# Optimization experiments

Measured on AMD Instinct MI355X. Metric: run time of the kernel, lower is better.

The kernel has to match this reference:

```python
import jax, jax.numpy as jnp
import numpy as np

WINDOW = 128  # crop size (compute_crops default window_size)


def centre_crop(centroids, window_size, h, w):
    # centroids: [C,2] int; returns flat gather coords [2, C*ws*ws]
    half = window_size // 2
    cy = jnp.clip(centroids[:, 0], half, h - half)
    cx = jnp.clip(centroids[:, 1], half, w - half)
    gy, gx = jnp.meshgrid(jnp.arange(window_size), jnp.arange(window_size), indexing='ij')
    rows = (cy - half)[:, None, None] + gy[None]  # [C,ws,ws]
    cols = (cx - half)[:, None, None] + gx[None]
    return jnp.stack([rows.reshape(-1), cols.reshape(-1)])  # [2, C*ws*ws]


def setup_inputs() -> dict:
    key = jax.random.key(0)
    ks = jax.random.split(key, 8)
    E, S, C, H, W = 6, 1, 512, 1024, 1024
    Dh = 16
    return {
        'x': jax.random.normal(ks[0], (E, H, W), dtype=jnp.float32),
        'sigma': jax.random.uniform(ks[1], (S, H, W), dtype=jnp.float32),
        'c': jax.random.normal(ks[2], (C, E), dtype=jnp.float32),
        'W1': jax.random.normal(ks[3], (E + S, Dh), dtype=jnp.float32) * 0.3,
        'b1': jnp.zeros((Dh,), dtype=jnp.float32),
        'W2': jax.random.normal(ks[4], (Dh, Dh), dtype=jnp.float32) * 0.3,
        'b2': jnp.zeros((Dh,), dtype=jnp.float32),
        'W3': jax.random.normal(ks[5], (Dh, 1), dtype=jnp.float32) * 0.3,
        'b3': jnp.zeros((1,), dtype=jnp.float32),
        'centroids_idx': jax.random.randint(ks[6], (C, 2), 0, H, dtype=jnp.int32),
    }


def reference(x, sigma, c, W1, b1, W2, b2, W3, b3, centroids_idx):
    E, h, w = x.shape
    S = sigma.shape[0]
    C = c.shape[0]
    ws = WINDOW
    mesh = centre_crop(centroids_idx, ws, h, w)  # [2, C*ws*ws]
    # gather per-instance windows from concatenated embedding+sigma maps
    xs = jnp.concatenate([x, sigma], axis=0)  # [E+S, H, W]
    g = xs[:, mesh[0], mesh[1]]               # [E+S, C*ws*ws]
    g = g.reshape(E + S, C, ws, ws).transpose(1, 0, 2, 3)  # [C, E+S, ws, ws]
    # subtract centroid descriptor from embedding channels (feature_engineering '0')
    g = jnp.concatenate([g[:, :E] - c[:, :, None, None], g[:, E:]], axis=1)
    feats = g.transpose(0, 2, 3, 1).reshape(-1, E + S)  # [(C*ws*ws), E+S]
    # per-pixel probability MLP (ProbabilityNet)
    hdn = jax.nn.relu(feats @ W1 + b1)
    hdn = jax.nn.relu(hdn @ W2 + b2)
    prob = jax.nn.sigmoid(hdn @ W3 + b3)
    prob = prob.reshape(C, 1, ws, ws)
    # instance-id / coordinate table for the downstream scatter (iidd)
    inst = jnp.repeat(jnp.arange(C, dtype=mesh.dtype), ws * ws)
    iidd = jnp.concatenate([inst[None], mesh], axis=0)  # [3, C*ws*ws]
    return prob, iidd
```

## Files before the change

### kernel.cpp

```cpp
#include <hip/hip_runtime.h>

#define WS 128
#define HW (1024 * 1024)
#define PLANE 8388608

typedef _Float16 half4 __attribute__((ext_vector_type(4)));
typedef _Float16 half8 __attribute__((ext_vector_type(8)));
typedef float floatx4 __attribute__((ext_vector_type(4)));

__global__ __launch_bounds__(256) void precompute_P(
    const float* __restrict__ x,
    const float* __restrict__ sigma,
    const float* __restrict__ W1,
    _Float16* __restrict__ P)
{
    const int px = blockIdx.x * 256 + threadIdx.x;
    float g[7];
#pragma unroll
    for (int e = 0; e < 6; ++e) g[e] = x[e * HW + px];
    g[6] = sigma[px];

    half8 lo, hi;
#pragma unroll
    for (int j = 0; j < 16; ++j) {
        float a = 0.0f;
#pragma unroll
        for (int e = 0; e < 7; ++e)
            a = fmaf(g[e], W1[e * 16 + j], a);
        if (j < 8) lo[j] = (_Float16)a; else hi[j - 8] = (_Float16)a;
    }
    *(half8*)(P + (size_t)px * 16)     = lo;
    *(half8*)(P + (size_t)px * 16 + 8) = hi;
}

__global__ __launch_bounds__(256) void instanseg_mlp(
    const _Float16* __restrict__ P,
    const float* __restrict__ c,
    const float* __restrict__ W1,
    const float* __restrict__ b1,
    const float* __restrict__ W2,
    const float* __restrict__ b2,
    const float* __restrict__ W3,
    const float* __restrict__ b3,
    const int*   __restrict__ cent,
    float* __restrict__ out)
{
    const int cid  = blockIdx.y;
    const int lane = threadIdx.x & 63;
    const int wave = threadIdx.x >> 6;
    const int quad = lane >> 4;
    const int sub  = lane & 15;

    const int cy = min(max(cent[2 * cid], 64), 960);
    const int cx = min(max(cent[2 * cid + 1], 64), 960);
    const int cy0 = cy - 64, cx0 = cx - 64;

    half4 a2;
    float w3f[4], bb2[4];
    half4 qh;
#pragma unroll
    for (int i = 0; i < 4; ++i) {
        const int k = 4 * quad + i;
        a2[i]  = (_Float16)W2[k * 16 + sub];
        w3f[i] = W3[k];
        bb2[i] = b2[k];
        float qv = -b1[k];
#pragma unroll
        for (int e = 0; e < 6; ++e)
            qv = fmaf(W1[e * 16 + k], c[cid * 6 + e], qv);
        qh[i] = (_Float16)qv;
    }
    const float b3v = b3[0];
    const floatx4 zero = {0.0f, 0.0f, 0.0f, 0.0f};

    const int wavestart = blockIdx.x * 2048 + wave * 512;

    for (int it = 0; it < 8; ++it) {
        const int start = wavestart + it * 64;
        float logit[4];
#pragma unroll
        for (int ch = 0; ch < 4; ++ch) {
            const int gp  = start + ch * 16 + sub;
            const int src = (cy0 + (gp >> 7)) * 1024 + cx0 + (gp & 127);

            half4 v = *(const half4*)(P + (size_t)src * 16 + quad * 4);
            half4 h = v - qh;
#pragma unroll
            for (int i = 0; i < 4; ++i)
                h[i] = h[i] > (_Float16)0.0f ? h[i] : (_Float16)0.0f;

            floatx4 c2 = __builtin_amdgcn_mfma_f32_16x16x16f16(a2, h, zero, 0, 0, 0);

            float part = 0.0f;
#pragma unroll
            for (int i = 0; i < 4; ++i)
                part = fmaf(w3f[i], fmaxf(c2[i] + bb2[i], 0.0f), part);
            part += __shfl_xor(part, 16, 64);
            part += __shfl_xor(part, 32, 64);
            logit[ch] = part;
        }

        const float l01 = (quad & 1) ? logit[1] : logit[0];
        const float l23 = (quad & 1) ? logit[3] : logit[2];
        const float lg  = (quad & 2) ? l23 : l01;
        const float prob = 1.0f / (1.0f + __expf(-(lg + b3v)));

        const int gps = start + lane;
        const int n   = cid * 16384 + gps;
        out[n]             = prob;
        out[PLANE + n]     = (float)cid;
        out[2 * PLANE + n] = (float)(cy0 + (gps >> 7));
        out[3 * PLANE + n] = (float)(cx0 + (gps & 127));
    }
}

extern "C" void kernel_launch(void* const* d_in, const int* in_sizes, int n_in,
                              void* d_out, int out_size, void* d_ws, size_t ws_size,
                              hipStream_t stream) {
    const float* x     = (const float*)d_in[0];
    const float* sigma = (const float*)d_in[1];
    const float* c     = (const float*)d_in[2];
    const float* W1    = (const float*)d_in[3];
    const float* b1    = (const float*)d_in[4];
    const float* W2    = (const float*)d_in[5];
    const float* b2    = (const float*)d_in[6];
    const float* W3    = (const float*)d_in[7];
    const float* b3    = (const float*)d_in[8];
    const int*   cent  = (const int*)d_in[9];
    float* out = (float*)d_out;
    _Float16* P = (_Float16*)d_ws;

    precompute_P<<<dim3(HW / 256), dim3(256), 0, stream>>>(x, sigma, W1, P);
    instanseg_mlp<<<dim3(8, 512), dim3(256), 0, stream>>>(
        P, c, W1, b1, W2, b2, W3, b3, cent, out);
}
```

Measured before the change: 211.8 us.

## Reorder crop blocks by Morton-sorted centroids for cache locality

An extra block added to the precompute kernel computes a Z-order key for each clamped centroid and ranks the 512 instances with an O(n^2) counting sort in shared memory. The MLP kernel now uses a 1D grid that maps each block to a sorted rank, interleaved across 8 groups, so spatially nearby crops run at about the same time and can share their P gathers in L2/MALL. The cost is the serial ranking block, which can lengthen the first kernel's tail, plus one extra indirection load per block. Output indexing still uses the original cid, so results stay correct.

```diff
diff --git a/kernel.cpp b/kernel.cpp
--- a/kernel.cpp
+++ b/kernel.cpp
@@ -3,17 +3,50 @@
 #define WS 128
 #define HW (1024 * 1024)
 #define PLANE 8388608
+#define PERM_BYTE_OFF 33554432
 
 typedef _Float16 half4 __attribute__((ext_vector_type(4)));
 typedef _Float16 half8 __attribute__((ext_vector_type(8)));
 typedef float floatx4 __attribute__((ext_vector_type(4)));
 
+__device__ inline unsigned part1by1(unsigned v) {
+    v &= 0x0000ffff;
+    v = (v ^ (v << 8)) & 0x00ff00ff;
+    v = (v ^ (v << 4)) & 0x0f0f0f0f;
+    v = (v ^ (v << 2)) & 0x33333333;
+    v = (v ^ (v << 1)) & 0x55555555;
+    return v;
+}
+
 __global__ __launch_bounds__(256) void precompute_P(
     const float* __restrict__ x,
     const float* __restrict__ sigma,
     const float* __restrict__ W1,
-    _Float16* __restrict__ P)
+    const int*   __restrict__ cent,
+    _Float16* __restrict__ P,
+    int* __restrict__ perm)
 {
+    if (blockIdx.x == 4096) {
+        __shared__ unsigned keys[512];
+        const int t = threadIdx.x;
+        for (int i = t; i < 512; i += 256) {
+            const unsigned cy = (unsigned)min(max(cent[2 * i], 64), 960);
+            const unsigned cx = (unsigned)min(max(cent[2 * i + 1], 64), 960);
+            keys[i] = (part1by1(cy) << 1) | part1by1(cx);
+        }
+        __syncthreads();
+        for (int i = t; i < 512; i += 256) {
+            const unsigned ki = keys[i];
+            int r = 0;
+            for (int j = 0; j < 512; ++j) {
+                const unsigned kj = keys[j];
+                r += (kj < ki || (kj == ki && j < i)) ? 1 : 0;
+            }
+            perm[r] = i;
+        }
+        return;
+    }
+
     const int px = blockIdx.x * 256 + threadIdx.x;
     float g[7];
 #pragma unroll
@@ -43,9 +76,16 @@
     const float* __restrict__ W3,
     const float* __restrict__ b3,
     const int*   __restrict__ cent,
+    const int*   __restrict__ perm,
     float* __restrict__ out)
 {
-    const int cid  = blockIdx.y;
+    const int lid   = blockIdx.x;
+    const int g     = lid & 7;
+    const int jj    = lid >> 3;
+    const int rank  = g * 64 + (jj >> 3);
+    const int chunk = jj & 7;
+    const int cid   = perm[rank];
+
     const int lane = threadIdx.x & 63;
     const int wave = threadIdx.x >> 6;
     const int quad = lane >> 4;
@@ -73,7 +113,7 @@
     const float b3v = b3[0];
     const floatx4 zero = {0.0f, 0.0f, 0.0f, 0.0f};
 
-    const int wavestart = blockIdx.x * 2048 + wave * 512;
+    const int wavestart = chunk * 2048 + wave * 512;
 
     for (int it = 0; it < 8; ++it) {
         const int start = wavestart + it * 64;
@@ -129,8 +169,9 @@
     const int*   cent  = (const int*)d_in[9];
     float* out = (float*)d_out;
     _Float16* P = (_Float16*)d_ws;
+    int* perm   = (int*)((char*)d_ws + PERM_BYTE_OFF);
 
-    precompute_P<<<dim3(HW / 256), dim3(256), 0, stream>>>(x, sigma, W1, P);
-    instanseg_mlp<<<dim3(8, 512), dim3(256), 0, stream>>>(
-        P, c, W1, b1, W2, b2, W3, b3, cent, out);
+    precompute_P<<<dim3(4097), dim3(256), 0, stream>>>(x, sigma, W1, cent, P, perm);
+    instanseg_mlp<<<dim3(4096), dim3(256), 0, stream>>>(
+        P, c, W1, b1, W2, b2, W3, b3, cent, perm, out);
 }
```

Result: slower. 218.8 us (+3.3%).

## Fuse W1 projection into tile-based MLP kernel with per-tile window lists

Applied to the files above, without the earlier changes.

Replaces the two-kernel scheme with one kernel. The old scheme wrote a full-image fp16 projection buffer to global memory and then re-gathered from it per crop window. Each block now owns a 32x32 image tile, builds a shared-memory list of the crop windows that overlap it, computes the W1 projection for the tile into LDS, and runs the MFMA MLP for every overlapping window from LDS. Outputs are written with nontemporal stores. This removes the global round trip of the projection buffer and the scattered gathers, but it adds per-tile load imbalance, since some tiles overlap many windows, partial wave utilisation at window edges, and strided output writes.

```diff
diff --git a/kernel.cpp b/kernel.cpp
--- a/kernel.cpp
+++ b/kernel.cpp
@@ -1,40 +1,16 @@
 #include <hip/hip_runtime.h>
 
-#define WS 128
 #define HW (1024 * 1024)
 #define PLANE 8388608
+#define TS 32
 
 typedef _Float16 half4 __attribute__((ext_vector_type(4)));
 typedef _Float16 half8 __attribute__((ext_vector_type(8)));
 typedef float floatx4 __attribute__((ext_vector_type(4)));
 
-__global__ __launch_bounds__(256) void precompute_P(
+__global__ __launch_bounds__(256) void instanseg_fused(
     const float* __restrict__ x,
     const float* __restrict__ sigma,
-    const float* __restrict__ W1,
-    _Float16* __restrict__ P)
-{
-    const int px = blockIdx.x * 256 + threadIdx.x;
-    float g[7];
-#pragma unroll
-    for (int e = 0; e < 6; ++e) g[e] = x[e * HW + px];
-    g[6] = sigma[px];
-
-    half8 lo, hi;
-#pragma unroll
-    for (int j = 0; j < 16; ++j) {
-        float a = 0.0f;
-#pragma unroll
-        for (int e = 0; e < 7; ++e)
-            a = fmaf(g[e], W1[e * 16 + j], a);
-        if (j < 8) lo[j] = (_Float16)a; else hi[j - 8] = (_Float16)a;
-    }
-    *(half8*)(P + (size_t)px * 16)     = lo;
-    *(half8*)(P + (size_t)px * 16 + 8) = hi;
-}
-
-__global__ __launch_bounds__(256) void instanseg_mlp(
-    const _Float16* __restrict__ P,
     const float* __restrict__ c,
     const float* __restrict__ W1,
     const float* __restrict__ b1,
@@ -45,72 +21,132 @@
     const int*   __restrict__ cent,
     float* __restrict__ out)
 {
-    const int cid  = blockIdx.y;
-    const int lane = threadIdx.x & 63;
-    const int wave = threadIdx.x >> 6;
-    const int quad = lane >> 4;
-    const int sub  = lane & 15;
+    __shared__ _Float16 tileP[TS * TS * 16];
+    __shared__ int wlist[512];
+    __shared__ int wcount;
 
-    const int cy = min(max(cent[2 * cid], 64), 960);
-    const int cx = min(max(cent[2 * cid + 1], 64), 960);
-    const int cy0 = cy - 64, cx0 = cx - 64;
+    const int tid = threadIdx.x;
+    const int ty = (blockIdx.x >> 5) * TS;
+    const int tx = (blockIdx.x & 31) * TS;
+
+    if (tid == 0) wcount = 0;
+    __syncthreads();
+
+    for (int w = tid; w < 512; w += 256) {
+        const int cy = min(max(cent[2 * w], 64), 960);
+        const int cx = min(max(cent[2 * w + 1], 64), 960);
+        const int cy0 = cy - 64, cx0 = cx - 64;
+        if (cy0 < ty + TS && cy0 + 128 > ty && cx0 < tx + TS && cx0 + 128 > tx)
+            wlist[atomicAdd(&wcount, 1)] = w;
+    }
+    __syncthreads();
+    const int nw = wcount;
+    if (nw == 0) return;
+
+#pragma unroll
+    for (int pass = 0; pass < 4; ++pass) {
+        const int p = pass * 256 + tid;
+        const int gpx = (ty + (p >> 5)) * 1024 + tx + (p & 31);
+        float g[7];
+#pragma unroll
+        for (int e = 0; e < 6; ++e) g[e] = x[e * HW + gpx];
+        g[6] = sigma[gpx];
+        half8 lo, hi;
+#pragma unroll
+        for (int j = 0; j < 16; ++j) {
+            float a = 0.0f;
+#pragma unroll
+            for (int e = 0; e < 7; ++e)
+                a = fmaf(g[e], W1[e * 16 + j], a);
+            if (j < 8) lo[j] = (_Float16)a; else hi[j - 8] = (_Float16)a;
+        }
+        *(half8*)&tileP[p * 16]     = lo;
+        *(half8*)&tileP[p * 16 + 8] = hi;
+    }
+    __syncthreads();
+
+    const int lane = tid & 63, wave = tid >> 6;
+    const int quad = lane >> 4, sub = lane & 15;
 
     half4 a2;
     float w3f[4], bb2[4];
-    half4 qh;
 #pragma unroll
     for (int i = 0; i < 4; ++i) {
         const int k = 4 * quad + i;
         a2[i]  = (_Float16)W2[k * 16 + sub];
         w3f[i] = W3[k];
         bb2[i] = b2[k];
-        float qv = -b1[k];
-#pragma unroll
-        for (int e = 0; e < 6; ++e)
-            qv = fmaf(W1[e * 16 + k], c[cid * 6 + e], qv);
-        qh[i] = (_Float16)qv;
     }
     const float b3v = b3[0];
     const floatx4 zero = {0.0f, 0.0f, 0.0f, 0.0f};
 
-    const int wavestart = blockIdx.x * 2048 + wave * 512;
+    for (int wi = 0; wi < nw; ++wi) {
+        const int cid = wlist[wi];
+        const int cy = min(max(cent[2 * cid], 64), 960);
+        const int cx = min(max(cent[2 * cid + 1], 64), 960);
+        const int cy0 = cy - 64, cx0 = cx - 64;
 
-    for (int it = 0; it < 8; ++it) {
-        const int start = wavestart + it * 64;
-        float logit[4];
+        half4 qh;
 #pragma unroll
-        for (int ch = 0; ch < 4; ++ch) {
-            const int gp  = start + ch * 16 + sub;
-            const int src = (cy0 + (gp >> 7)) * 1024 + cx0 + (gp & 127);
-
-            half4 v = *(const half4*)(P + (size_t)src * 16 + quad * 4);
-            half4 h = v - qh;
+        for (int i = 0; i < 4; ++i) {
+            const int k = 4 * quad + i;
+            float qv = -b1[k];
 #pragma unroll
-            for (int i = 0; i < 4; ++i)
-                h[i] = h[i] > (_Float16)0.0f ? h[i] : (_Float16)0.0f;
-
-            floatx4 c2 = __builtin_amdgcn_mfma_f32_16x16x16f16(a2, h, zero, 0, 0, 0);
-
-            float part = 0.0f;
-#pragma unroll
-            for (int i = 0; i < 4; ++i)
-                part = fmaf(w3f[i], fmaxf(c2[i] + bb2[i], 0.0f), part);
-            part += __shfl_xor(part, 16, 64);
-            part += __shfl_xor(part, 32, 64);
-            logit[ch] = part;
+            for (int e = 0; e < 6; ++e)
+                qv = fmaf(W1[e * 16 + k], c[cid * 6 + e], qv);
+            qh[i] = (_Float16)qv;
         }
 
-        const float l01 = (quad & 1) ? logit[1] : logit[0];
-        const float l23 = (quad & 1) ? logit[3] : logit[2];
-        const float lg  = (quad & 2) ? l23 : l01;
-        const float prob = 1.0f / (1.0f + __expf(-(lg + b3v)));
+        const int r0 = max(cy0 - ty, 0), r1 = min(cy0 + 128 - ty, TS);
+        const int c0 = max(cx0 - tx, 0), c1 = min(cx0 + 128 - tx, TS);
+        const int c0a  = c0 & ~15;
+        const int segw = (c1 - c0a + 15) >> 4;
+        const int rpi  = (segw == 2) ? 2 : 4;
 
-        const int gps = start + lane;
-        const int n   = cid * 16384 + gps;
-        out[n]             = prob;
-        out[PLANE + n]     = (float)cid;
-        out[2 * PLANE + n] = (float)(cy0 + (gps >> 7));
-        out[3 * PLANE + n] = (float)(cx0 + (gps & 127));
+        for (int rb = r0 + wave * rpi; rb < r1; rb += rpi * 4) {
+            float logit[4];
+#pragma unroll
+            for (int ch = 0; ch < 4; ++ch) {
+                const int dr  = (segw == 2) ? (ch >> 1) : ch;
+                const int cs  = (segw == 2) ? (ch & 1) : 0;
+                const int row = rb + dr;
+                const int rc  = min(row, TS - 1);
+                const int lc  = c0a + cs * 16 + sub;
+                half4 v = *(const half4*)&tileP[(rc * TS + lc) * 16 + quad * 4];
+                half4 h = v - qh;
+#pragma unroll
+                for (int i = 0; i < 4; ++i)
+                    h[i] = h[i] > (_Float16)0.0f ? h[i] : (_Float16)0.0f;
+
+                floatx4 c2 = __builtin_amdgcn_mfma_f32_16x16x16f16(a2, h, zero, 0, 0, 0);
+
+                float part = 0.0f;
+#pragma unroll
+                for (int i = 0; i < 4; ++i)
+                    part = fmaf(w3f[i], fmaxf(c2[i] + bb2[i], 0.0f), part);
+                part += __shfl_xor(part, 16, 64);
+                part += __shfl_xor(part, 32, 64);
+                logit[ch] = part;
+            }
+
+            const float l01 = (quad & 1) ? logit[1] : logit[0];
+            const float l23 = (quad & 1) ? logit[3] : logit[2];
+            const float lg  = (quad & 2) ? l23 : l01;
+
+            const int dr_l  = (segw == 2) ? (quad >> 1) : quad;
+            const int cs_l  = (segw == 2) ? (quad & 1) : 0;
+            const int row_l = rb + dr_l;
+            const int lc_l  = c0a + cs_l * 16 + sub;
+            if (row_l < r1 && lc_l >= c0 && lc_l < c1) {
+                const float prob = 1.0f / (1.0f + __expf(-(lg + b3v)));
+                const int iy = ty + row_l, ix = tx + lc_l;
+                const int n  = cid * 16384 + (iy - cy0) * 128 + (ix - cx0);
+                __builtin_nontemporal_store(prob,        out + n);
+                __builtin_nontemporal_store((float)cid,  out + PLANE + n);
+                __builtin_nontemporal_store((float)iy,   out + 2 * PLANE + n);
+                __builtin_nontemporal_store((float)ix,   out + 3 * PLANE + n);
+            }
+        }
     }
 }
 
@@ -128,9 +164,8 @@
     const float* b3    = (const float*)d_in[8];
     const int*   cent  = (const int*)d_in[9];
     float* out = (float*)d_out;
-    _Float16* P = (_Float16*)d_ws;
+    (void)d_ws; (void)ws_size;
 
-    precompute_P<<<dim3(HW / 256), dim3(256), 0, stream>>>(x, sigma, W1, P);
-    instanseg_mlp<<<dim3(8, 512), dim3(256), 0, stream>>>(
-        P, c, W1, b1, W2, b2, W3, b3, cent, out);
+    instanseg_fused<<<dim3(1024), dim3(256), 0, stream>>>(
+        x, sigma, c, W1, b1, W2, b2, W3, b3, cent, out);
 }
```

New measurement: 292.3 us. 1.38x slower.

## Store packed fp16 inputs instead of precomputed layer-1 outputs and apply W1 via MFMA

Applied to the files above, without the earlier changes.

The precompute pass now writes only the 7 input channels (padded to 8) as fp16 per pixel, instead of the 16 first-layer activations. The main kernel applies W1 with an extra 16x16x16 MFMA per chunk, then subtracts the centroid term in fp32. This halves the intermediate buffer written and gathered, from 32 to 16 bytes per pixel, at the cost of one more matrix instruction per chunk. Inputs are now rounded to fp16 before the first layer, which changes precision slightly.

```diff
diff --git a/kernel.cpp b/kernel.cpp
--- a/kernel.cpp
+++ b/kernel.cpp
@@ -8,33 +8,22 @@
 typedef _Float16 half8 __attribute__((ext_vector_type(8)));
 typedef float floatx4 __attribute__((ext_vector_type(4)));
 
-__global__ __launch_bounds__(256) void precompute_P(
+__global__ __launch_bounds__(256) void precompute_G(
     const float* __restrict__ x,
     const float* __restrict__ sigma,
-    const float* __restrict__ W1,
-    _Float16* __restrict__ P)
+    _Float16* __restrict__ G)
 {
     const int px = blockIdx.x * 256 + threadIdx.x;
-    float g[7];
+    half8 g;
 #pragma unroll
-    for (int e = 0; e < 6; ++e) g[e] = x[e * HW + px];
-    g[6] = sigma[px];
-
-    half8 lo, hi;
-#pragma unroll
-    for (int j = 0; j < 16; ++j) {
-        float a = 0.0f;
-#pragma unroll
-        for (int e = 0; e < 7; ++e)
-            a = fmaf(g[e], W1[e * 16 + j], a);
-        if (j < 8) lo[j] = (_Float16)a; else hi[j - 8] = (_Float16)a;
-    }
-    *(half8*)(P + (size_t)px * 16)     = lo;
-    *(half8*)(P + (size_t)px * 16 + 8) = hi;
+    for (int e = 0; e < 6; ++e) g[e] = (_Float16)x[e * HW + px];
+    g[6] = (_Float16)sigma[px];
+    g[7] = (_Float16)0.0f;
+    *(half8*)(G + (size_t)px * 8) = g;
 }
 
 __global__ __launch_bounds__(256) void instanseg_mlp(
-    const _Float16* __restrict__ P,
+    const _Float16* __restrict__ G,
     const float* __restrict__ c,
     const float* __restrict__ W1,
     const float* __restrict__ b1,
@@ -55,9 +44,15 @@
     const int cx = min(max(cent[2 * cid + 1], 64), 960);
     const int cy0 = cy - 64, cx0 = cx - 64;
 
+    half4 a1;
+#pragma unroll
+    for (int i = 0; i < 4; ++i) {
+        const int k = 4 * quad + i;
+        a1[i] = (k < 7) ? (_Float16)W1[k * 16 + sub] : (_Float16)0.0f;
+    }
+
     half4 a2;
-    float w3f[4], bb2[4];
-    half4 qh;
+    float w3f[4], bb2[4], qf[4];
 #pragma unroll
     for (int i = 0; i < 4; ++i) {
         const int k = 4 * quad + i;
@@ -68,7 +63,7 @@
 #pragma unroll
         for (int e = 0; e < 6; ++e)
             qv = fmaf(W1[e * 16 + k], c[cid * 6 + e], qv);
-        qh[i] = (_Float16)qv;
+        qf[i] = qv;
     }
     const float b3v = b3[0];
     const floatx4 zero = {0.0f, 0.0f, 0.0f, 0.0f};
@@ -83,11 +78,16 @@
             const int gp  = start + ch * 16 + sub;
             const int src = (cy0 + (gp >> 7)) * 1024 + cx0 + (gp & 127);
 
-            half4 v = *(const half4*)(P + (size_t)src * 16 + quad * 4);
-            half4 h = v - qh;
+            half4 bg = {};
+            if (quad < 2)
+                bg = *(const half4*)(G + (size_t)src * 8 + quad * 4);
+
+            floatx4 c1 = __builtin_amdgcn_mfma_f32_16x16x16f16(a1, bg, zero, 0, 0, 0);
+
+            half4 h;
 #pragma unroll
             for (int i = 0; i < 4; ++i)
-                h[i] = h[i] > (_Float16)0.0f ? h[i] : (_Float16)0.0f;
+                h[i] = (_Float16)fmaxf(c1[i] - qf[i], 0.0f);
 
             floatx4 c2 = __builtin_amdgcn_mfma_f32_16x16x16f16(a2, h, zero, 0, 0, 0);
 
@@ -128,9 +128,9 @@
     const float* b3    = (const float*)d_in[8];
     const int*   cent  = (const int*)d_in[9];
     float* out = (float*)d_out;
-    _Float16* P = (_Float16*)d_ws;
+    _Float16* G = (_Float16*)d_ws;
 
-    precompute_P<<<dim3(HW / 256), dim3(256), 0, stream>>>(x, sigma, W1, P);
+    precompute_G<<<dim3(HW / 256), dim3(256), 0, stream>>>(x, sigma, G);
     instanseg_mlp<<<dim3(8, 512), dim3(256), 0, stream>>>(
-        P, c, W1, b1, W2, b2, W3, b3, cent, out);
+        G, c, W1, b1, W2, b2, W3, b3, cent, out);
 }
```

Result: faster. 201.0 us (-5.1%).
